# Kernel optimization log

Measured on AMD Instinct MI355X. Metric: run time of the kernel, lower is better.

Reference implementation:

```python
import jax, jax.numpy as jnp
import numpy as np
from jax import lax


def _maxpool_same(x, k):
    # stride-1 max pool with symmetric padding p=(k-1)//2, pad value -inf
    # (matches torch max_pool2d implicit -inf padding)
    p = (k - 1) // 2
    return lax.reduce_window(
        x,
        -jnp.inf,
        lax.max,
        window_dimensions=(1, 1, k, k),
        window_strides=(1, 1, 1, 1),
        padding=[(0, 0), (0, 0), (p, p), (p, p)],
    )


def setup_inputs() -> dict:
    key = jax.random.key(0)
    x = jax.random.normal(key, (16, 256, 64, 64), dtype=jnp.float32)
    return {"x": x}


def reference(x):
    # SPP: concat(x, maxpool5(x), maxpool9(x), maxpool13(x)) along channels
    x1 = _maxpool_same(x, 5)
    x2 = _maxpool_same(x, 9)
    x3 = _maxpool_same(x, 13)
    return jnp.concatenate([x, x1, x2, x3], axis=1)  # [B, 4C, H, W]
```

## Files before the change

### kernel.cpp

```cpp
#include <hip/hip_runtime.h>
#include <math.h>

#define TPB 256
#define W 64
#define H 64
#define LDSW 68

__global__ __launch_bounds__(TPB) void spp_kernel(const float* __restrict__ in,
                                                  float* __restrict__ out) {
    __shared__ __align__(16) float s_r5[H * LDSW];

    const int tid  = threadIdx.x;
    const int lane = tid & 63;
    const int bc   = blockIdx.x;
    const int b    = bc >> 8;
    const int c    = bc & 255;
    const size_t img   = (size_t)bc * (H * W);
    const size_t obase = ((size_t)b * 1024 + c) * (H * W);
    const size_t pstr  = (size_t)256 * H * W;
    const float NEG = -INFINITY;

    {
        const float4* in4 = (const float4*)(in + img);
        float4* o4 = (float4*)(out + obase);
        const int  lm1 = (lane - 1) & 63;
        const int  lp1 = (lane + 1) & 63;
        const bool qlo = (lane & 15) == 0;
        const bool qhi = (lane & 15) == 15;
        #pragma unroll
        for (int i = 0; i < 4; ++i) {
            const int idx = tid + TPB * i;
            float4 v = in4[idx];
            o4[idx] = v;
            float e0 = __shfl(v.z, lm1, 64);
            float e1 = __shfl(v.w, lm1, 64);
            float e6 = __shfl(v.x, lp1, 64);
            float e7 = __shfl(v.y, lp1, 64);
            if (qlo) { e0 = NEG; e1 = NEG; }
            if (qhi) { e6 = NEG; e7 = NEG; }
            const float e2 = v.x, e3 = v.y, e4 = v.z, e5 = v.w;
            const float p0 = fmaxf(e0, e1), p1 = fmaxf(e1, e2), p2 = fmaxf(e2, e3);
            const float p3 = fmaxf(e3, e4), p4 = fmaxf(e4, e5), p5 = fmaxf(e5, e6);
            float4 r;
            r.x = fmaxf(fmaxf(p0, p2), e4);
            r.y = fmaxf(fmaxf(p1, p3), e5);
            r.z = fmaxf(fmaxf(p2, p4), e6);
            r.w = fmaxf(fmaxf(p3, p5), e7);
            const int y = idx >> 4;
            const int q = idx & 15;
            *(float4*)&s_r5[y * LDSW + 4 * q] = r;
        }
    }
    __syncthreads();

    {
        const int x  = lane;
        const int y0 = (tid >> 6) << 4;
        float cv[28];
        #pragma unroll
        for (int j = 0; j < 28; ++j) {
            const int y = y0 - 6 + j;
            cv[j] = (y >= 0 && y < H) ? s_r5[y * LDSW + x] : NEG;
        }
        float p2a[27], p4a[25], p8a[21];
        #pragma unroll
        for (int j = 0; j < 27; ++j) p2a[j] = fmaxf(cv[j], cv[j + 1]);
        #pragma unroll
        for (int j = 0; j < 25; ++j) p4a[j] = fmaxf(p2a[j], p2a[j + 2]);
        #pragma unroll
        for (int j = 0; j < 21; ++j) p8a[j] = fmaxf(p4a[j], p4a[j + 4]);

        const int xm2 = (x >= 2)  ? x - 2 : 0;
        const int xp2 = (x <= 61) ? x + 2 : 63;
        const int xm4 = (x >= 4)  ? x - 4 : 0;
        const int xp4 = (x <= 59) ? x + 4 : 63;

        float* o5  = out + obase +     pstr + x;
        float* o9  = out + obase + 2 * pstr + x;
        float* o13 = out + obase + 3 * pstr + x;
        #pragma unroll
        for (int i = 0; i < 16; ++i) {
            const float c5  = fmaxf(p4a[i + 4], cv[i + 8]);
            const float c9  = fmaxf(p8a[i + 2], cv[i + 10]);
            const float c13 = fmaxf(p8a[i], fmaxf(p4a[i + 8], cv[i + 12]));

            o5[(y0 + i) * W] = c5;

            const float a9 = __shfl(c9, xm2, 64);
            const float b9 = __shfl(c9, xp2, 64);
            o9[(y0 + i) * W] = fmaxf(a9, b9);

            const float a13 = __shfl(c13, xm4, 64);
            const float b13 = __shfl(c13, xp4, 64);
            o13[(y0 + i) * W] = fmaxf(fmaxf(a13, c13), b13);
        }
    }
}

extern "C" void kernel_launch(void* const* d_in, const int* in_sizes, int n_in,
                              void* d_out, int out_size, void* d_ws, size_t ws_size,
                              hipStream_t stream) {
    const float* x = (const float*)d_in[0];
    float* out = (float*)d_out;
    spp_kernel<<<dim3(4096), dim3(TPB), 0, stream>>>(x, out);
}
```

Baseline: 312.1 us.

## Process two images per block with software-pipelined loads and nontemporal memory ops

Each block now handles two channel images. It issues the second image's global loads before running the column and output phase of the first image, using two LDS buffers so the two phases can overlap. All global loads and stores become nontemporal, so the streaming traffic bypasses cache retention. The grid is halved and the launch_bounds hint is dropped, which may raise register pressure and lower occupancy. LDS use per block doubles.

```diff
diff --git a/kernel.cpp b/kernel.cpp
--- a/kernel.cpp
+++ b/kernel.cpp
@@ -6,95 +6,118 @@
 #define H 64
 #define LDSW 68
 
-__global__ __launch_bounds__(TPB) void spp_kernel(const float* __restrict__ in,
-                                                  float* __restrict__ out) {
-    __shared__ __align__(16) float s_r5[H * LDSW];
+typedef float f32x4 __attribute__((ext_vector_type(4)));
+
+__device__ __forceinline__ void p1_rest(const f32x4 v[4], float* __restrict__ s,
+                                        float* __restrict__ outimg, int tid) {
+    const int  lane = tid & 63;
+    const int  lm1 = (lane - 1) & 63;
+    const int  lp1 = (lane + 1) & 63;
+    const bool qlo = (lane & 15) == 0;
+    const bool qhi = (lane & 15) == 15;
+    const float NEG = -INFINITY;
+    f32x4* o4 = (f32x4*)outimg;
+    #pragma unroll
+    for (int i = 0; i < 4; ++i) {
+        const int idx = tid + TPB * i;
+        f32x4 t = v[i];
+        __builtin_nontemporal_store(t, o4 + idx);
+        float e0 = __shfl(t.z, lm1, 64);
+        float e1 = __shfl(t.w, lm1, 64);
+        float e6 = __shfl(t.x, lp1, 64);
+        float e7 = __shfl(t.y, lp1, 64);
+        if (qlo) { e0 = NEG; e1 = NEG; }
+        if (qhi) { e6 = NEG; e7 = NEG; }
+        const float e2 = t.x, e3 = t.y, e4 = t.z, e5 = t.w;
+        const float p0 = fmaxf(e0, e1), p1 = fmaxf(e1, e2), p2 = fmaxf(e2, e3);
+        const float p3 = fmaxf(e3, e4), p4 = fmaxf(e4, e5), p5 = fmaxf(e5, e6);
+        f32x4 r;
+        r.x = fmaxf(fmaxf(p0, p2), e4);
+        r.y = fmaxf(fmaxf(p1, p3), e5);
+        r.z = fmaxf(fmaxf(p2, p4), e6);
+        r.w = fmaxf(fmaxf(p3, p5), e7);
+        const int y = idx >> 4;
+        const int q = idx & 15;
+        *(f32x4*)&s[y * LDSW + 4 * q] = r;
+    }
+}
+
+__device__ __forceinline__ void p2(const float* __restrict__ s,
+                                   float* __restrict__ outimg, int tid) {
+    const float NEG = -INFINITY;
+    const size_t pstr = (size_t)256 * H * W;
+    const int x  = tid & 63;
+    const int y0 = (tid >> 6) << 4;
+    float cv[28];
+    #pragma unroll
+    for (int j = 0; j < 28; ++j) {
+        const int y = y0 - 6 + j;
+        cv[j] = (y >= 0 && y < H) ? s[y * LDSW + x] : NEG;
+    }
+    float p2a[27], p4a[25], p8a[21];
+    #pragma unroll
+    for (int j = 0; j < 27; ++j) p2a[j] = fmaxf(cv[j], cv[j + 1]);
+    #pragma unroll
+    for (int j = 0; j < 25; ++j) p4a[j] = fmaxf(p2a[j], p2a[j + 2]);
+    #pragma unroll
+    for (int j = 0; j < 21; ++j) p8a[j] = fmaxf(p4a[j], p4a[j + 4]);
+
+    const int xm2 = (x >= 2)  ? x - 2 : 0;
+    const int xp2 = (x <= 61) ? x + 2 : 63;
+    const int xm4 = (x >= 4)  ? x - 4 : 0;
+    const int xp4 = (x <= 59) ? x + 4 : 63;
+
+    float* o5  = outimg +     pstr + x;
+    float* o9  = outimg + 2 * pstr + x;
+    float* o13 = outimg + 3 * pstr + x;
+    #pragma unroll
+    for (int i = 0; i < 16; ++i) {
+        const float c5  = fmaxf(p4a[i + 4], cv[i + 8]);
+        const float c9  = fmaxf(p8a[i + 2], cv[i + 10]);
+        const float c13 = fmaxf(p8a[i], fmaxf(p4a[i + 8], cv[i + 12]));
+
+        __builtin_nontemporal_store(c5, o5 + (y0 + i) * W);
+
+        const float a9 = __shfl(c9, xm2, 64);
+        const float b9 = __shfl(c9, xp2, 64);
+        __builtin_nontemporal_store(fmaxf(a9, b9), o9 + (y0 + i) * W);
+
+        const float a13 = __shfl(c13, xm4, 64);
+        const float b13 = __shfl(c13, xp4, 64);
+        __builtin_nontemporal_store(fmaxf(fmaxf(a13, c13), b13), o13 + (y0 + i) * W);
+    }
+}
+
+__global__ void spp_kernel(const float* __restrict__ in, float* __restrict__ out) {
+    __shared__ __align__(16) float s_a[H * LDSW];
+    __shared__ __align__(16) float s_b[H * LDSW];
 
     const int tid  = threadIdx.x;
-    const int lane = tid & 63;
-    const int bc   = blockIdx.x;
-    const int b    = bc >> 8;
-    const int c    = bc & 255;
-    const size_t img   = (size_t)bc * (H * W);
-    const size_t obase = ((size_t)b * 1024 + c) * (H * W);
-    const size_t pstr  = (size_t)256 * H * W;
-    const float NEG = -INFINITY;
+    const int imgA = blockIdx.x * 2;
+    const int imgB = imgA + 1;
+    const size_t obaseA = (((size_t)(imgA >> 8)) * 1024 + (imgA & 255)) * (H * W);
+    const size_t obaseB = (((size_t)(imgB >> 8)) * 1024 + (imgB & 255)) * (H * W);
 
+    f32x4 va[4];
     {
-        const float4* in4 = (const float4*)(in + img);
-        float4* o4 = (float4*)(out + obase);
-        const int  lm1 = (lane - 1) & 63;
-        const int  lp1 = (lane + 1) & 63;
-        const bool qlo = (lane & 15) == 0;
-        const bool qhi = (lane & 15) == 15;
+        const f32x4* in4 = (const f32x4*)(in + (size_t)imgA * (H * W));
         #pragma unroll
-        for (int i = 0; i < 4; ++i) {
-            const int idx = tid + TPB * i;
-            float4 v = in4[idx];
-            o4[idx] = v;
-            float e0 = __shfl(v.z, lm1, 64);
-            float e1 = __shfl(v.w, lm1, 64);
-            float e6 = __shfl(v.x, lp1, 64);
-            float e7 = __shfl(v.y, lp1, 64);
-            if (qlo) { e0 = NEG; e1 = NEG; }
-            if (qhi) { e6 = NEG; e7 = NEG; }
-            const float e2 = v.x, e3 = v.y, e4 = v.z, e5 = v.w;
-            const float p0 = fmaxf(e0, e1), p1 = fmaxf(e1, e2), p2 = fmaxf(e2, e3);
-            const float p3 = fmaxf(e3, e4), p4 = fmaxf(e4, e5), p5 = fmaxf(e5, e6);
-            float4 r;
-            r.x = fmaxf(fmaxf(p0, p2), e4);
-            r.y = fmaxf(fmaxf(p1, p3), e5);
-            r.z = fmaxf(fmaxf(p2, p4), e6);
-            r.w = fmaxf(fmaxf(p3, p5), e7);
-            const int y = idx >> 4;
-            const int q = idx & 15;
-            *(float4*)&s_r5[y * LDSW + 4 * q] = r;
-        }
+        for (int i = 0; i < 4; ++i) va[i] = __builtin_nontemporal_load(in4 + tid + TPB * i);
     }
+    p1_rest(va, s_a, out + obaseA, tid);
     __syncthreads();
 
+    f32x4 vb[4];
     {
-        const int x  = lane;
-        const int y0 = (tid >> 6) << 4;
-        float cv[28];
+        const f32x4* in4 = (const f32x4*)(in + (size_t)imgB * (H * W));
         #pragma unroll
-        for (int j = 0; j < 28; ++j) {
-            const int y = y0 - 6 + j;
-            cv[j] = (y >= 0 && y < H) ? s_r5[y * LDSW + x] : NEG;
-        }
-        float p2a[27], p4a[25], p8a[21];
-        #pragma unroll
-        for (int j = 0; j < 27; ++j) p2a[j] = fmaxf(cv[j], cv[j + 1]);
-        #pragma unroll
-        for (int j = 0; j < 25; ++j) p4a[j] = fmaxf(p2a[j], p2a[j + 2]);
-        #pragma unroll
-        for (int j = 0; j < 21; ++j) p8a[j] = fmaxf(p4a[j], p4a[j + 4]);
+        for (int i = 0; i < 4; ++i) vb[i] = __builtin_nontemporal_load(in4 + tid + TPB * i);
+    }
+    p2(s_a, out + obaseA, tid);
+    p1_rest(vb, s_b, out + obaseB, tid);
+    __syncthreads();
 
-        const int xm2 = (x >= 2)  ? x - 2 : 0;
-        const int xp2 = (x <= 61) ? x + 2 : 63;
-        const int xm4 = (x >= 4)  ? x - 4 : 0;
-        const int xp4 = (x <= 59) ? x + 4 : 63;
-
-        float* o5  = out + obase +     pstr + x;
-        float* o9  = out + obase + 2 * pstr + x;
-        float* o13 = out + obase + 3 * pstr + x;
-        #pragma unroll
-        for (int i = 0; i < 16; ++i) {
-            const float c5  = fmaxf(p4a[i + 4], cv[i + 8]);
-            const float c9  = fmaxf(p8a[i + 2], cv[i + 10]);
-            const float c13 = fmaxf(p8a[i], fmaxf(p4a[i + 8], cv[i + 12]));
-
-            o5[(y0 + i) * W] = c5;
-
-            const float a9 = __shfl(c9, xm2, 64);
-            const float b9 = __shfl(c9, xp2, 64);
-            o9[(y0 + i) * W] = fmaxf(a9, b9);
-
-            const float a13 = __shfl(c13, xm4, 64);
-            const float b13 = __shfl(c13, xp4, 64);
-            o13[(y0 + i) * W] = fmaxf(fmaxf(a13, c13), b13);
-        }
-    }
+    p2(s_b, out + obaseB, tid);
 }
 
 extern "C" void kernel_launch(void* const* d_in, const int* in_sizes, int n_in,
@@ -102,5 +125,5 @@
                               hipStream_t stream) {
     const float* x = (const float*)d_in[0];
     float* out = (float*)d_out;
-    spp_kernel<<<dim3(4096), dim3(TPB), 0, stream>>>(x, out);
+    spp_kernel<<<dim3(2048), dim3(TPB), 0, stream>>>(x, out);
 }
```

Measured after the change: 309.7 us. Within noise of the previous version (-0.8%).
